# Kernel optimization log

Measured on AMD Instinct MI355X. Metric: run time of the kernel, lower is better.

Reference implementation:

```python
import jax, jax.numpy as jnp
import numpy as np

IN_F = 128   # in_features
INTER, CMD, MOT = 135, 89, 32   # AutoNCP(256, 32) layer sizes
OUT = 32     # out_features
B, T = 256, 1024


def setup_inputs() -> dict:
    key = jax.random.key(0)
    ks = jax.random.split(key, 32)

    def lin(k, o, i):
        s = 1.0 / np.sqrt(i)
        kw, kb = jax.random.split(k)
        w = jax.random.uniform(kw, (o, i), minval=-s, maxval=s, dtype=jnp.float32)
        b = jax.random.uniform(kb, (o,), minval=-s, maxval=s, dtype=jnp.float32)
        return w, b

    inp = {"x": jax.random.normal(ks[0], (B, T, IN_F), dtype=jnp.float32)}
    sizes = [(INTER, IN_F), (CMD, INTER), (MOT, CMD)]  # (units, layer_input)
    i = 1
    for li, (u, fin) in enumerate(sizes):
        cat = fin + u
        for nm in ["ff1", "ff2", "ta", "tb"]:
            w, b = lin(ks[i], u, cat); i += 1
            inp[f"l{li}_{nm}_w"] = w
            inp[f"l{li}_{nm}_b"] = b
        # NCP sparsity mask: random 0/1 on layer-input block, all-ones on recurrent block
        m_in = jax.random.randint(ks[i], (u, fin), 0, 2, dtype=jnp.int32); i += 1
        inp[f"mask{li}"] = jnp.concatenate([m_in, jnp.ones((u, u), jnp.int32)], axis=1)
    w, b = lin(ks[i], OUT, OUT)
    inp["fc_w"] = w
    inp["fc_b"] = b
    return inp


def _cfc_cell(z_in, h, ff1_w, ff1_b, ff2_w, ff2_b, ta_w, ta_b, tb_w, tb_b, mask):
    # CfCCell, mode='default', backbone_layers=0, ts=1.0
    z = jnp.concatenate([z_in, h], axis=-1)            # [B, in+u]
    ff1 = jnp.tanh(z @ (ff1_w * mask).T + ff1_b)
    ff2 = jnp.tanh(z @ (ff2_w * mask).T + ff2_b)
    t_interp = jax.nn.sigmoid((z @ ta_w.T + ta_b) * 1.0 + (z @ tb_w.T + tb_b))
    return ff1 * (1.0 - t_interp) + t_interp * ff2


def _adaptive_avg_pool1d(x, out_size):
    # pools last dim (torch AdaptiveAvgPool1d semantics)
    L = x.shape[-1]
    i = jnp.arange(out_size)
    starts = (i * L) // out_size
    ends = ((i + 1) * L + out_size - 1) // out_size
    idx = jnp.arange(L)
    m = ((idx[None, :] >= starts[:, None]) & (idx[None, :] < ends[:, None])).astype(x.dtype)
    m = m / (ends - starts)[:, None].astype(x.dtype)   # [out, L]
    return x @ m.T


def _forward(x,
             l0_ff1_w, l0_ff1_b, l0_ff2_w, l0_ff2_b, l0_ta_w, l0_ta_b, l0_tb_w, l0_tb_b,
             l1_ff1_w, l1_ff1_b, l1_ff2_w, l1_ff2_b, l1_ta_w, l1_ta_b, l1_tb_w, l1_tb_b,
             l2_ff1_w, l2_ff1_b, l2_ff2_w, l2_ff2_b, l2_ta_w, l2_ta_b, l2_tb_w, l2_tb_b,
             fc_w, fc_b, mask0, mask1, mask2):
    dt = x.dtype
    p0 = (l0_ff1_w, l0_ff1_b, l0_ff2_w, l0_ff2_b, l0_ta_w, l0_ta_b, l0_tb_w, l0_tb_b, mask0.astype(dt))
    p1 = (l1_ff1_w, l1_ff1_b, l1_ff2_w, l1_ff2_b, l1_ta_w, l1_ta_b, l1_tb_w, l1_tb_b, mask1.astype(dt))
    p2 = (l2_ff1_w, l2_ff1_b, l2_ff2_w, l2_ff2_b, l2_ta_w, l2_ta_b, l2_tb_w, l2_tb_b, mask2.astype(dt))
    Bx = x.shape[0]
    h_init = (jnp.zeros((Bx, INTER), dt), jnp.zeros((Bx, CMD), dt), jnp.zeros((Bx, MOT), dt))

    def step(carry, xt):
        h0, h1, h2 = carry
        h0 = _cfc_cell(xt, h0, *p0)   # inter layer
        h1 = _cfc_cell(h0, h1, *p1)   # command layer
        h2 = _cfc_cell(h1, h2, *p2)   # motor layer (sequence output)
        return (h0, h1, h2), h2

    _, ys = jax.lax.scan(step, h_init, jnp.swapaxes(x, 0, 1))  # ys: [T, B, MOT]
    seq = jnp.swapaxes(ys, 0, 1)                               # [B, T, MOT]
    pooled = _adaptive_avg_pool1d(seq, OUT)                    # identity when MOT == OUT
    return pooled @ fc_w.T + fc_b


def reference(x,
              l0_ff1_w, l0_ff1_b, l0_ff2_w, l0_ff2_b, l0_ta_w, l0_ta_b, l0_tb_w, l0_tb_b,
              l1_ff1_w, l1_ff1_b, l1_ff2_w, l1_ff2_b, l1_ta_w, l1_ta_b, l1_tb_w, l1_tb_b,
              l2_ff1_w, l2_ff1_b, l2_ff2_w, l2_ff2_b, l2_ta_w, l2_ta_b, l2_tb_w, l2_tb_b,
              fc_w, fc_b, mask0, mask1, mask2):
    return _forward(x,
                    l0_ff1_w, l0_ff1_b, l0_ff2_w, l0_ff2_b, l0_ta_w, l0_ta_b, l0_tb_w, l0_tb_b,
                    l1_ff1_w, l1_ff1_b, l1_ff2_w, l1_ff2_b, l1_ta_w, l1_ta_b, l1_tb_w, l1_tb_b,
                    l2_ff1_w, l2_ff1_b, l2_ff2_w, l2_ff2_b, l2_ta_w, l2_ta_b, l2_tb_w, l2_tb_b,
                    fc_w, fc_b, mask0, mask1, mask2)
```

## Files before the change

kernel.cpp:

```cpp
#include <hip/hip_runtime.h>
#include <cmath>


constexpr int TT   = 1024;
constexpr int NB   = 256;
constexpr int GRP  = 32;
constexpr int WPG  = 8;
constexpr int CAT0 = 263, CAT1 = 224, CAT2 = 121;
constexpr int U0P = 136, U1P = 92, U2P = 32;

constexpr int ZP   = 272;
constexpr int CH   = 68;
constexpr int ZB0s = 0;
constexpr int ZB1s = 8 * ZP;
constexpr int ZB2s = 16 * ZP;
constexpr int ZTOT = 24 * ZP;
constexpr int SMEM_BYTES = ZTOT * 4;

constexpr int HBLK   = 8*U0P + 8*U1P + 8*U2P;
constexpr int SEG1   = 8*U0P;
constexpr int SEG2   = SEG1 + 8*U1P;
constexpr int FLAG_OFF = 2 * GRP * HBLK;
constexpr int WS_DW    = FLAG_OFF + GRP * 16;

typedef float f2 __attribute__((ext_vector_type(2)));

struct Params {
  const float* x;
  const float* w[3][4];
  const float* b[3][4];
  const int*   mk[3];
  float* hx;
  int*   flags;
  float* out;
};

__device__ __forceinline__ void sysstore(float* p, float v) {
  __hip_atomic_store(p, v, __ATOMIC_RELAXED, __HIP_MEMORY_SCOPE_SYSTEM);
}
__device__ __forceinline__ float4 cload(const float4* p) {
  float4 v;
  asm volatile("global_load_dwordx4 %0, %1, off sc0 sc1"
               : "=v"(v) : "v"(p) : "memory");
  return v;
}
__device__ __forceinline__ void cwait() {
  asm volatile("s_waitcnt vmcnt(0)" ::: "memory");
}
__device__ __forceinline__ float frcp(float x) { return __builtin_amdgcn_rcpf(x); }
__device__ __forceinline__ float ftanh(float x) {
  const float e = __expf(-2.f * fabsf(x));
  return copysignf((1.f - e) * frcp(1.f + e), x);
}

extern "C" __global__ void __launch_bounds__(256, 1)
lnn_main(Params p) {
  extern __shared__ float smem[];
  const int tid   = threadIdx.x;
  const int g     = blockIdx.x & 31;
  const int w_idx = blockIdx.x >> 5;

  const int n0  = (w_idx < 7) ? 17 : 16;
  const int us0 = w_idx * 17;
  const int n1  = (w_idx < 7) ? 11 : 12;
  const int us1 = w_idx * 11;
  const int us2 = w_idx * 4;

  const int cp   = tid >> 2;
  const int q    = tid & 3;
  const int tsel = cp & 1;
  const int s    = cp >> 1;
  int lyr, u_loc;
  if (s < n0)           { lyr = 0; u_loc = s; }
  else if (s < n0 + n1) { lyr = 1; u_loc = s - n0; }
  else                  { lyr = 2; u_loc = s - n0 - n1; }
  const int ug  = (lyr == 0) ? us0 + u_loc : (lyr == 1) ? us1 + u_loc : us2 + u_loc;
  const int cat = (lyr == 0) ? CAT0 : (lyr == 1) ? CAT1 : CAT2;
  const int zb  = (lyr == 0) ? ZB0s : (lyr == 1) ? ZB1s : ZB2s;
  const int seg = (lyr == 0) ? 0 : (lyr == 1) ? SEG1 : SEG2;
  const int UP  = (lyr == 0) ? U0P : (lyr == 1) ? U1P : U2P;
  const int zoff = zb + q * CH;
  const int b0 = q & 1, b1 = (q >> 1) & 1;
  const int rA = 2 * q;

  f2 wAl[17], wAh[17], wBl[17], wBh[17];
  {
    const float* gwA = p.w[lyr][tsel * 2]     + (size_t)ug * cat;
    const float* gwB = p.w[lyr][tsel * 2 + 1] + (size_t)ug * cat;
    const int*   gmk = p.mk[lyr]              + (size_t)ug * cat;
    const int k0 = q * CH;
    #pragma unroll
    for (int i = 0; i < 17; ++i) {
      float va[4], vb[4];
      #pragma unroll
      for (int e = 0; e < 4; ++e) {
        const int k = k0 + i * 4 + e;
        int src;
        if (lyr == 0)      src = (k < 263) ? k : -1;
        else if (lyr == 1) src = (k < 135) ? k : (k >= 136 && k < 225) ? k - 1 : -1;
        else               src = (k < 89)  ? k : (k >= 92  && k < 124) ? k - 3 : -1;
        float a = 0.f, b = 0.f;
        if (src >= 0) {
          a = gwA[src]; b = gwB[src];
          if (tsel == 0) { const float mm = (float)gmk[src]; a *= mm; b *= mm; }
        }
        va[e] = a; vb[e] = b;
      }
      wAl[i] = (f2){va[0], va[1]}; wAh[i] = (f2){va[2], va[3]};
      wBl[i] = (f2){vb[0], vb[1]}; wBh[i] = (f2){vb[2], vb[3]};
    }
  }
  const float bias0 = p.b[lyr][tsel * 2][ug];
  const float bias1 = p.b[lyr][tsel * 2 + 1][ug];

  for (int i = tid; i < ZTOT; i += 256) smem[i] = 0.f;
  __syncthreads();

  for (int k = 0; k < TT + 3; ++k) {
    const int p0 = (k - 1) & 1;
    const int p1 = k & 1;

    const float4* hx0 = (const float4*)(p.hx + (size_t)(p0 * GRP + g) * HBLK);
    const float4* hx1 = (const float4*)(p.hx + (size_t)(p1 * GRP + g) * HBLK);
    const int i1 = tid + 256;
    const float4 hv0 = cload(hx0 + tid);
    const float4 hv1 = cload((i1 >= 272 && i1 < 456) ? hx1 + i1 : hx0 + i1);
    float4 hvt;
    if (tid < 8) hvt = cload(hx0 + 512 + tid);

    const int tx = (k < TT) ? k : TT - 1;
    {
      const int r = tid >> 5, c4 = (tid & 31) * 4;
      const float4 v = *(const float4*)(p.x + ((size_t)(g * 8 + r) * TT + tx) * 128 + c4);
      *(float4*)(&smem[r * ZP + c4]) = v;
    }

    cwait();

    {
      const int r = tid / 34, c4 = (tid - r * 34) * 4;
      *(float4*)(&smem[r * ZP + 128 + c4]) = hv0;
      *(float4*)(&smem[ZB1s + r * ZP + c4]) = hv0;
    }
    if (i1 < 272) {
      const int r = i1 / 34, c4 = (i1 - r * 34) * 4;
      *(float4*)(&smem[r * ZP + 128 + c4]) = hv1;
      *(float4*)(&smem[ZB1s + r * ZP + c4]) = hv1;
    } else if (i1 < 456) {
      const int j = i1 - 272;
      const int r = j / 23, c4 = (j - r * 23) * 4;
      *(float4*)(&smem[ZB1s + r * ZP + 136 + c4]) = hv1;
      *(float4*)(&smem[ZB2s + r * ZP + c4]) = hv1;
    } else {
      const int j = i1 - 456;
      const int r = j >> 3, c4 = (j & 7) * 4;
      *(float4*)(&smem[ZB2s + r * ZP + 92 + c4]) = hv1;
    }
    if (tid < 8) {
      const int j = tid + 56;
      const int r = j >> 3, c4 = (j & 7) * 4;
      *(float4*)(&smem[ZB2s + r * ZP + 92 + c4]) = hvt;
    }
    __syncthreads();

    if (tid < 8 && k >= 3) {
      const float4 v = *(const float4*)(&smem[ZB2s + w_idx * ZP + 92 + tid * 4]);
      *(float4*)(&p.out[((size_t)(g * 8 + w_idx) * TT + (k - 3)) * 32 + tid * 4]) = v;
    }

    f2 accA[8], accB[8];
    #pragma unroll
    for (int r = 0; r < 8; ++r) { accA[r] = (f2){0.f, 0.f}; accB[r] = (f2){0.f, 0.f}; }
    {
      const float* zp = &smem[zoff];
      #pragma unroll
      for (int i = 0; i < 17; ++i) {
        #pragma unroll
        for (int r = 0; r < 8; ++r) {
          const float4 a = *(const float4*)(zp + r * ZP + i * 4);
          const f2 al = {a.x, a.y}, ah = {a.z, a.w};
          accA[r] = __builtin_elementwise_fma(al, wAl[i], accA[r]);
          accB[r] = __builtin_elementwise_fma(al, wBl[i], accB[r]);
          accA[r] = __builtin_elementwise_fma(ah, wAh[i], accA[r]);
          accB[r] = __builtin_elementwise_fma(ah, wBh[i], accB[r]);
        }
      }
    }

    float acc[8][2];
    #pragma unroll
    for (int r = 0; r < 8; ++r) {
      float u0 = accA[r].x + accA[r].y;
      float u1 = accB[r].x + accB[r].y;
      u0 += __shfl_xor(u0, 1);  u0 += __shfl_xor(u0, 2);
      u1 += __shfl_xor(u1, 1);  u1 += __shfl_xor(u1, 2);
      acc[r][0] = u0; acc[r][1] = u1;
    }

    const float v00 = (b1 ? (b0 ? acc[6][0] : acc[4][0]) : (b0 ? acc[2][0] : acc[0][0])) + bias0;
    const float v01 = (b1 ? (b0 ? acc[6][1] : acc[4][1]) : (b0 ? acc[2][1] : acc[0][1])) + bias1;
    const float v10 = (b1 ? (b0 ? acc[7][0] : acc[5][0]) : (b0 ? acc[3][0] : acc[1][0])) + bias0;
    const float v11 = (b1 ? (b0 ? acc[7][1] : acc[5][1]) : (b0 ? acc[3][1] : acc[1][1])) + bias1;

    float sA = v00 + v01, sB = v10 + v11;
    sA = frcp(1.f + __expf(-sA));
    sB = frcp(1.f + __expf(-sB));
    const float gA = __shfl_down(sA, 4);
    const float gB = __shfl_down(sB, 4);
    if (tsel == 0) {
      const float hA = ftanh(v00) * (1.f - gA) + gA * ftanh(v01);
      const float hB = ftanh(v10) * (1.f - gB) + gB * ftanh(v11);
      const int tl = k - lyr;
      if (tl >= 0 && tl < TT) {
        float* dst = p.hx + (size_t)((tl & 1) * GRP + g) * HBLK + seg + ug;
        sysstore(dst + (size_t)rA * UP, hA);
        sysstore(dst + (size_t)(rA + 1) * UP, hB);
      }
    }

    __syncthreads();
    if (tid == 0)
      __hip_atomic_store(&p.flags[g * 16 + w_idx], k + 1,
                         __ATOMIC_RELAXED, __HIP_MEMORY_SCOPE_SYSTEM);
    if (k < TT + 2) {
      if (tid < WPG) {
        const int* fp = &p.flags[g * 16 + tid];
        while (__hip_atomic_load(fp, __ATOMIC_RELAXED, __HIP_MEMORY_SCOPE_SYSTEM) < k + 1)
          __builtin_amdgcn_s_sleep(1);
      }
      __syncthreads();
    }
  }
}

extern "C" __global__ void __launch_bounds__(256)
lnn_fc(float* out, const float* fcw, const float* fcb) {
  __shared__ float w[32 * 33];
  __shared__ float bb[32];
  __shared__ float tile[8 * 32];
  const int tid = threadIdx.x;
  for (int i = tid; i < 1024; i += 256) w[(i >> 5) * 33 + (i & 31)] = fcw[i];
  if (tid < 32) bb[tid] = fcb[tid];
  const size_t base = (size_t)blockIdx.x * 256;
  tile[tid] = out[base + tid];
  __syncthreads();
  const int pp = tid >> 5, o = tid & 31;
  float acc = bb[o];
  #pragma unroll
  for (int u = 0; u < 32; ++u) acc = fmaf(tile[pp * 32 + u], w[o * 33 + u], acc);
  out[base + pp * 32 + o] = acc;
}

extern "C" void kernel_launch(void* const* d_in, const int* in_sizes, int n_in,
                              void* d_out, int out_size, void* d_ws, size_t ws_size,
                              hipStream_t stream) {
  Params p;
  p.x = (const float*)d_in[0];
  const int wi[3] = {1, 10, 19};
  for (int l = 0; l < 3; ++l) {
    for (int m = 0; m < 4; ++m) {
      p.w[l][m] = (const float*)d_in[wi[l] + 2 * m];
      p.b[l][m] = (const float*)d_in[wi[l] + 2 * m + 1];
    }
  }
  p.mk[0] = (const int*)d_in[9];
  p.mk[1] = (const int*)d_in[18];
  p.mk[2] = (const int*)d_in[27];
  float* ws = (float*)d_ws;
  p.hx    = ws;
  p.flags = (int*)(ws + FLAG_OFF);
  p.out   = (float*)d_out;

  hipFuncSetAttribute(reinterpret_cast<const void*>(lnn_main),
                      hipFuncAttributeMaxDynamicSharedMemorySize, SMEM_BYTES);
  hipMemsetAsync(d_ws, 0, (size_t)WS_DW * 4, stream);
  lnn_main<<<dim3(GRP * WPG), dim3(256), SMEM_BYTES, stream>>>(p);
  lnn_fc<<<dim3(NB * TT / 8), dim3(256), 0, stream>>>(
      (float*)d_out, (const float*)d_in[28], (const float*)d_in[29]);
}
```

Before: 4.815 ms.

## Fold time-gate weights into one matrix and remap threads to eight per unit

The ta and tb weight matrices and biases are summed once at load time, since the reference adds the two projections before the sigmoid. This cuts the per-step matvec work from four projections to three. Threads are regrouped so that eight lanes share one unit, each covering 36 padded columns and computing all three projections. The row padding grows to 288. Partial sums are reduced with lane shuffles plus a shared-memory exchange between the two half-groups, which adds a block barrier and a scratch buffer to every step in exchange for fewer FMAs and less register-held weight duplication.

```diff
diff --git a/kernel.cpp b/kernel.cpp
--- a/kernel.cpp
+++ b/kernel.cpp
@@ -9,13 +9,14 @@
 constexpr int CAT0 = 263, CAT1 = 224, CAT2 = 121;
 constexpr int U0P = 136, U1P = 92, U2P = 32;
 
-constexpr int ZP   = 272;
-constexpr int CH   = 68;
+constexpr int ZP   = 288;
 constexpr int ZB0s = 0;
 constexpr int ZB1s = 8 * ZP;
 constexpr int ZB2s = 16 * ZP;
 constexpr int ZTOT = 24 * ZP;
-constexpr int SMEM_BYTES = ZTOT * 4;
+constexpr int SCR  = ZTOT;
+constexpr int SMEM_DW    = ZTOT + 256 * 4;
+constexpr int SMEM_BYTES = SMEM_DW * 4;
 
 constexpr int HBLK   = 8*U0P + 8*U1P + 8*U2P;
 constexpr int SEG1   = 8*U0P;
@@ -66,10 +67,8 @@
   const int us1 = w_idx * 11;
   const int us2 = w_idx * 4;
 
-  const int cp   = tid >> 2;
-  const int q    = tid & 3;
-  const int tsel = cp & 1;
-  const int s    = cp >> 1;
+  const int q8 = tid & 7;
+  const int s  = tid >> 3;
   int lyr, u_loc;
   if (s < n0)           { lyr = 0; u_loc = s; }
   else if (s < n0 + n1) { lyr = 1; u_loc = s - n0; }
@@ -79,19 +78,18 @@
   const int zb  = (lyr == 0) ? ZB0s : (lyr == 1) ? ZB1s : ZB2s;
   const int seg = (lyr == 0) ? 0 : (lyr == 1) ? SEG1 : SEG2;
   const int UP  = (lyr == 0) ? U0P : (lyr == 1) ? U1P : U2P;
-  const int zoff = zb + q * CH;
-  const int b0 = q & 1, b1 = (q >> 1) & 1;
-  const int rA = 2 * q;
-
-  f2 wAl[17], wAh[17], wBl[17], wBh[17];
+  const int k0  = q8 * 36;
+
+  f2 w0l[9], w0h[9], w1l[9], w1h[9], w2l[9], w2h[9];
   {
-    const float* gwA = p.w[lyr][tsel * 2]     + (size_t)ug * cat;
-    const float* gwB = p.w[lyr][tsel * 2 + 1] + (size_t)ug * cat;
-    const int*   gmk = p.mk[lyr]              + (size_t)ug * cat;
-    const int k0 = q * CH;
+    const float* gw0 = p.w[lyr][0] + (size_t)ug * cat;
+    const float* gw1 = p.w[lyr][1] + (size_t)ug * cat;
+    const float* gw2 = p.w[lyr][2] + (size_t)ug * cat;
+    const float* gw3 = p.w[lyr][3] + (size_t)ug * cat;
+    const int*   gmk = p.mk[lyr]   + (size_t)ug * cat;
     #pragma unroll
-    for (int i = 0; i < 17; ++i) {
-      float va[4], vb[4];
+    for (int i = 0; i < 9; ++i) {
+      float v0[4], v1[4], v2[4];
       #pragma unroll
       for (int e = 0; e < 4; ++e) {
         const int k = k0 + i * 4 + e;
@@ -99,19 +97,23 @@
         if (lyr == 0)      src = (k < 263) ? k : -1;
         else if (lyr == 1) src = (k < 135) ? k : (k >= 136 && k < 225) ? k - 1 : -1;
         else               src = (k < 89)  ? k : (k >= 92  && k < 124) ? k - 3 : -1;
-        float a = 0.f, b = 0.f;
+        float a = 0.f, b = 0.f, c = 0.f;
         if (src >= 0) {
-          a = gwA[src]; b = gwB[src];
-          if (tsel == 0) { const float mm = (float)gmk[src]; a *= mm; b *= mm; }
+          const float mm = (float)gmk[src];
+          a = gw0[src] * mm;
+          b = gw1[src] * mm;
+          c = gw2[src] + gw3[src];
         }
-        va[e] = a; vb[e] = b;
+        v0[e] = a; v1[e] = b; v2[e] = c;
       }
-      wAl[i] = (f2){va[0], va[1]}; wAh[i] = (f2){va[2], va[3]};
-      wBl[i] = (f2){vb[0], vb[1]}; wBh[i] = (f2){vb[2], vb[3]};
+      w0l[i] = (f2){v0[0], v0[1]}; w0h[i] = (f2){v0[2], v0[3]};
+      w1l[i] = (f2){v1[0], v1[1]}; w1h[i] = (f2){v1[2], v1[3]};
+      w2l[i] = (f2){v2[0], v2[1]}; w2h[i] = (f2){v2[2], v2[3]};
     }
   }
-  const float bias0 = p.b[lyr][tsel * 2][ug];
-  const float bias1 = p.b[lyr][tsel * 2 + 1][ug];
+  const float bf1 = p.b[lyr][0][ug];
+  const float bf2 = p.b[lyr][1][ug];
+  const float bt  = p.b[lyr][2][ug] + p.b[lyr][3][ug];
 
   for (int i = tid; i < ZTOT; i += 256) smem[i] = 0.f;
   __syncthreads();
@@ -168,54 +170,45 @@
       *(float4*)(&p.out[((size_t)(g * 8 + w_idx) * TT + (k - 3)) * 32 + tid * 4]) = v;
     }
 
-    f2 accA[8], accB[8];
-    #pragma unroll
-    for (int r = 0; r < 8; ++r) { accA[r] = (f2){0.f, 0.f}; accB[r] = (f2){0.f, 0.f}; }
+    float own0 = 0.f, own1 = 0.f, own2 = 0.f;
+    float giv0 = 0.f, giv1 = 0.f, giv2 = 0.f;
     {
-      const float* zp = &smem[zoff];
+      const float* zp = &smem[zb + k0];
       #pragma unroll
-      for (int i = 0; i < 17; ++i) {
+      for (int r = 0; r < 8; ++r) {
+        f2 a0 = {0.f, 0.f}, a1 = {0.f, 0.f}, a2 = {0.f, 0.f};
         #pragma unroll
-        for (int r = 0; r < 8; ++r) {
-          const float4 a = *(const float4*)(zp + r * ZP + i * 4);
-          const f2 al = {a.x, a.y}, ah = {a.z, a.w};
-          accA[r] = __builtin_elementwise_fma(al, wAl[i], accA[r]);
-          accB[r] = __builtin_elementwise_fma(al, wBl[i], accB[r]);
-          accA[r] = __builtin_elementwise_fma(ah, wAh[i], accA[r]);
-          accB[r] = __builtin_elementwise_fma(ah, wBh[i], accB[r]);
+        for (int i = 0; i < 9; ++i) {
+          const float4 z4 = *(const float4*)(zp + r * ZP + i * 4);
+          const f2 zl = {z4.x, z4.y}, zh = {z4.z, z4.w};
+          a0 = __builtin_elementwise_fma(zl, w0l[i], a0);
+          a1 = __builtin_elementwise_fma(zl, w1l[i], a1);
+          a2 = __builtin_elementwise_fma(zl, w2l[i], a2);
+          a0 = __builtin_elementwise_fma(zh, w0h[i], a0);
+          a1 = __builtin_elementwise_fma(zh, w1h[i], a1);
+          a2 = __builtin_elementwise_fma(zh, w2h[i], a2);
         }
+        float u0 = a0.x + a0.y, u1 = a1.x + a1.y, u2 = a2.x + a2.y;
+        u0 += __shfl_xor(u0, 1);  u0 += __shfl_xor(u0, 2);
+        u1 += __shfl_xor(u1, 1);  u1 += __shfl_xor(u1, 2);
+        u2 += __shfl_xor(u2, 1);  u2 += __shfl_xor(u2, 2);
+        if (r == q8)       { own0 = u0; own1 = u1; own2 = u2; }
+        if (r == (q8 ^ 4)) { giv0 = u0; giv1 = u1; giv2 = u2; }
       }
     }
-
-    float acc[8][2];
-    #pragma unroll
-    for (int r = 0; r < 8; ++r) {
-      float u0 = accA[r].x + accA[r].y;
-      float u1 = accB[r].x + accB[r].y;
-      u0 += __shfl_xor(u0, 1);  u0 += __shfl_xor(u0, 2);
-      u1 += __shfl_xor(u1, 1);  u1 += __shfl_xor(u1, 2);
-      acc[r][0] = u0; acc[r][1] = u1;
-    }
-
-    const float v00 = (b1 ? (b0 ? acc[6][0] : acc[4][0]) : (b0 ? acc[2][0] : acc[0][0])) + bias0;
-    const float v01 = (b1 ? (b0 ? acc[6][1] : acc[4][1]) : (b0 ? acc[2][1] : acc[0][1])) + bias1;
-    const float v10 = (b1 ? (b0 ? acc[7][0] : acc[5][0]) : (b0 ? acc[3][0] : acc[1][0])) + bias0;
-    const float v11 = (b1 ? (b0 ? acc[7][1] : acc[5][1]) : (b0 ? acc[3][1] : acc[1][1])) + bias1;
-
-    float sA = v00 + v01, sB = v10 + v11;
-    sA = frcp(1.f + __expf(-sA));
-    sB = frcp(1.f + __expf(-sB));
-    const float gA = __shfl_down(sA, 4);
-    const float gB = __shfl_down(sB, 4);
-    if (tsel == 0) {
-      const float hA = ftanh(v00) * (1.f - gA) + gA * ftanh(v01);
-      const float hB = ftanh(v10) * (1.f - gB) + gB * ftanh(v11);
-      const int tl = k - lyr;
-      if (tl >= 0 && tl < TT) {
-        float* dst = p.hx + (size_t)((tl & 1) * GRP + g) * HBLK + seg + ug;
-        sysstore(dst + (size_t)rA * UP, hA);
-        sysstore(dst + (size_t)(rA + 1) * UP, hB);
-      }
+    *(float4*)(&smem[SCR + tid * 4]) = (float4){giv0, giv1, giv2, 0.f};
+    __syncthreads();
+    const float4 par = *(const float4*)(&smem[SCR + (tid ^ 4) * 4]);
+
+    const float F1 = own0 + par.x + bf1;
+    const float F2 = own1 + par.y + bf2;
+    const float T  = own2 + par.z + bt;
+    const float t  = frcp(1.f + __expf(-T));
+    const float h  = ftanh(F1) * (1.f - t) + t * ftanh(F2);
+    const int   tl = k - lyr;
+    if (tl >= 0 && tl < TT) {
+      float* dst = p.hx + (size_t)((tl & 1) * GRP + g) * HBLK + seg + ug;
+      sysstore(dst + (size_t)q8 * UP, h);
     }
 
     __syncthreads();
```

Result: faster. 4.512 ms (-6.3%).
